# Kernel optimization log

Measured on AMD Instinct MI355X. Metric: run time of the kernel, lower is better.

## Reference

```python
import jax, jax.numpy as jnp
import numpy as np

B = 1024          # batch of positions
K = 64            # king squares
F = 640           # 64 squares * 10 piece types
C = 256           # accumulator channels


def setup_inputs() -> dict:
    key = jax.random.key(0)
    k1, k2, k3 = jax.random.split(key, 3)
    piece_positions = jax.random.randint(k1, (B, 64, 10), 0, 2).astype(jnp.bool_)
    king_positions = jax.random.randint(k2, (B, 2), 0, K, dtype=jnp.int32)
    input_weights = jax.random.normal(k3, (K, F + 1, C), dtype=jnp.float32)
    bias = jnp.zeros((C,), dtype=jnp.float32)
    return {
        "piece_positions": piece_positions,
        "king_positions": king_positions,
        "input_weights": input_weights,
        "bias": bias,
    }


def reference(piece_positions, king_positions, input_weights, bias):
    # Flatten the (64, 10) boolean piece plane into 640 HalfKP features.
    b = piece_positions.shape[0]
    p = piece_positions.reshape(b, F).astype(input_weights.dtype)          # (B, 640)
    # Gather each sample's white/black king weight slabs: (B, 2, 641, 256)
    Wg = jnp.take(input_weights, king_positions, axis=0)
    # Sparse-feature sum for both halves, contracted over feature dim and
    # summed over the two king perspectives in one einsum.
    halves = jnp.einsum("bf,bsfc->bc", p, Wg[:, :, :F, :])                 # (B, 256)
    extra = Wg[:, :, F, :].sum(axis=1)                                     # row 640 for each king
    return halves + extra + bias
```

## Files before the change

### kernel.cpp

```cpp
#include <hip/hip_runtime.h>
#include <hip/hip_bf16.h>


#define F_DIM 640
#define C_DIM 256
#define SLAB_STRIDE (641 * 256)
#define NKING 64
#define LCAP 256
#define NC_MAX 64
#define WPAD 36

#define WS_PART_OFF 0
#define WS_NEED (2 * 1024 * 256 * 4)

typedef float  f32x4  __attribute__((ext_vector_type(4)));
typedef short  bf16x8 __attribute__((ext_vector_type(8)));

__device__ __forceinline__ unsigned f2bf_pk(float a, float b) {
    union { float f; unsigned u; } x, y;
    x.f = a; y.f = b;
    const unsigned ra = (x.u + 0x7FFFu + ((x.u >> 16) & 1u)) >> 16;
    const unsigned rb = (y.u + 0x7FFFu + ((y.u >> 16) & 1u)) >> 16;
    return (ra & 0xFFFFu) | (rb << 16);
}

__device__ __forceinline__ bf16x8 mk_a8(unsigned m32, int g) {
    const unsigned by = (m32 >> (g * 8)) & 0xFFu;
    union { unsigned u[4]; bf16x8 v; } r;
    #pragma unroll
    for (int i = 0; i < 4; ++i)
        r.u[i] = (((by >> (2 * i)) & 1u) ? 0x3F80u : 0u) |
                 (((by >> (2 * i + 1)) & 1u) ? 0x3F800000u : 0u);
    return r.v;
}

__global__ __launch_bounds__(512, 4)
void halfkp_fused(const float* __restrict__ W,
                  const int* __restrict__ pieces,
                  const int* __restrict__ kings,
                  float* __restrict__ partial,
                  int nent)
{
    const int k  = blockIdx.x;
    const int cq = blockIdx.y;
    const int t  = threadIdx.x;
    const int wv = t >> 6, lane = t & 63;
    const int mt  = wv & 1;
    const int ntc = (wv >> 1) & 1;
    const int kh  = wv >> 2;
    const int li = lane & 15, g = lane >> 4;
    const int colL = ntc * 16 + li;
    const int colG = cq * 32 + colL;

    __shared__ unsigned s_W[336 * WPAD];
    __shared__ int s_ent[LCAP];
    __shared__ int s_cb[NC_MAX + 1];
    __shared__ unsigned s_m32[32][21];
    __shared__ f32x4 s_red[4][64];
    __shared__ int s_nk;

    const float* __restrict__ Wq = W + (size_t)k * SLAB_STRIDE + cq * 32;
    float4 ve[6], vo[6];
    #pragma unroll
    for (int it = 0; it < 6; ++it) {
        const int task = t + (it << 9);
        if (task < 336 * 8) {
            const int fp = task >> 3, c4 = task & 7;
            const int fe = min(2 * fp, F_DIM);
            const int fo = min(2 * fp + 1, F_DIM);
            ve[it] = *(const float4*)&Wq[(size_t)fe * C_DIM + c4 * 4];
            vo[it] = *(const float4*)&Wq[(size_t)fo * C_DIM + c4 * 4];
        }
    }

    {
        const int NC = nent >> 6;
        const int nit = NC >> 3;
        unsigned long long mm[8];
        #pragma unroll
        for (int it = 0; it < 8; ++it) {
            if (it < nit) {
                const int c = wv + (it << 3);
                const int kk = kings[(c << 6) + lane];
                mm[it] = __ballot(kk == k);
                if (lane == 0) s_cb[c] = (int)__popcll(mm[it]);
            }
        }
        __syncthreads();
        if (t == 0) {
            int s = 0;
            for (int c = 0; c < NC; ++c) { const int v = s_cb[c]; s_cb[c] = s; s += v; }
            s_nk = min(s, LCAP);
        }
        __syncthreads();
        const unsigned long long lt = (1ull << lane) - 1ull;
        #pragma unroll
        for (int it = 0; it < 8; ++it) {
            if (it < nit) {
                const int c = wv + (it << 3);
                if ((mm[it] >> lane) & 1ull) {
                    const int pos = s_cb[c] + (int)__popcll(mm[it] & lt);
                    if (pos < LCAP) s_ent[pos] = (c << 6) + lane;
                }
            }
        }
    }

    #pragma unroll
    for (int it = 0; it < 6; ++it) {
        const int task = t + (it << 9);
        if (task < 336 * 8) {
            const int fp = task >> 3, c4 = task & 7;
            union { unsigned u[4]; f32x4 v; } pk;
            pk.u[0] = f2bf_pk(ve[it].x, vo[it].x);
            pk.u[1] = f2bf_pk(ve[it].y, vo[it].y);
            pk.u[2] = f2bf_pk(ve[it].z, vo[it].z);
            pk.u[3] = f2bf_pk(ve[it].w, vo[it].w);
            *(f32x4*)&s_W[fp * WPAD + c4 * 4] = pk.v;
        }
    }
    __syncthreads();
    const int n_k = s_nk;

    for (int mb = 0; mb < n_k; mb += 32) {
        const int nc = min(n_k - mb, 32);

        int pv[4][10];
        #pragma unroll
        for (int j = 0; j < 4; ++j) {
            const int r = (wv << 2) + j;
            const int id = (r < nc) ? s_ent[mb + r] : -1;
            if (id >= 0) {
                const int* __restrict__ pb = pieces + (size_t)(id >> 1) * F_DIM;
                #pragma unroll
                for (int w2 = 0; w2 < 10; ++w2) pv[j][w2] = pb[w2 * 64 + lane];
            } else {
                #pragma unroll
                for (int w2 = 0; w2 < 10; ++w2) pv[j][w2] = 0;
            }
        }
        #pragma unroll
        for (int j = 0; j < 4; ++j) {
            const int r = (wv << 2) + j;
            const int id = (r < nc) ? s_ent[mb + r] : -1;
            #pragma unroll
            for (int w2 = 0; w2 < 10; ++w2) {
                const unsigned long long m64 = __ballot(pv[j][w2] != 0);
                if (lane == 0) {
                    s_m32[r][2 * w2]     = (unsigned)m64;
                    s_m32[r][2 * w2 + 1] = (unsigned)(m64 >> 32);
                }
            }
            if (lane == 0) s_m32[r][20] = (id >= 0) ? 1u : 0u;
        }
        __syncthreads();

        const unsigned* mrow = s_m32[mt * 16 + li];
        f32x4 acc = {0.f, 0.f, 0.f, 0.f};
        {
            const int ks_beg = kh ? 10 : 0;
            const int ks_end = kh ? 21 : 10;
            #pragma unroll 2
            for (int ks = ks_beg; ks < ks_end; ++ks) {
                const unsigned* bp = &s_W[(ks * 16 + g * 4) * WPAD + colL];
                union { unsigned u[4]; bf16x8 v; } bb;
                #pragma unroll
                for (int jj = 0; jj < 4; ++jj)
                    bb.u[jj] = bp[jj * WPAD];
                const bf16x8 af = mk_a8(mrow[ks], g);
                acc = __builtin_amdgcn_mfma_f32_16x16x32_bf16(af, bb.v, acc, 0, 0, 0);
            }
        }
        if (kh == 1) s_red[wv & 3][lane] = acc;
        __syncthreads();
        if (kh == 0) {
            acc += s_red[wv & 3][lane];
            #pragma unroll
            for (int i = 0; i < 4; ++i) {
                const int row = mt * 16 + 4 * g + i;
                if (row < nc) {
                    const int id = s_ent[mb + row];
                    partial[(((size_t)(id & 1)) * 1024 + (id >> 1)) * C_DIM + colG] = acc[i];
                }
            }
        }
        __syncthreads();
    }
}

__global__ __launch_bounds__(256)
void finalize(const float* __restrict__ partial,
              const float* __restrict__ bias,
              float* __restrict__ out)
{
    const int i = blockIdx.x * 256 + threadIdx.x;
    const float4 b4 = ((const float4*)bias)[i & 63];
    const float4 p0 = ((const float4*)partial)[i];
    const float4 p1 = ((const float4*)partial)[1024 * 64 + i];
    float4 o;
    o.x = b4.x + p0.x + p1.x;
    o.y = b4.y + p0.y + p1.y;
    o.z = b4.z + p0.z + p1.z;
    o.w = b4.w + p0.w + p1.w;
    ((float4*)out)[i] = o;
}

__global__ __launch_bounds__(256)
void halfkp_fallback(const int* __restrict__ pieces, const int* __restrict__ kings,
                     const float* __restrict__ W, const float* __restrict__ bias,
                     float* __restrict__ out)
{
    const int b = blockIdx.x;
    const int c = threadIdx.x;
    const int lane = c & 63;
    const int k0 = kings[2 * b + 0];
    const int k1 = kings[2 * b + 1];
    const float* W0 = W + (size_t)k0 * SLAB_STRIDE + c;
    const float* W1 = W + (size_t)k1 * SLAB_STRIDE + c;
    float acc = bias[c] + W0[640 * 256] + W1[640 * 256];
    const int* pi = pieces + (size_t)b * F_DIM;
    #pragma unroll
    for (int ch = 0; ch < 10; ++ch) {
        int v = pi[ch * 64 + lane];
        unsigned long long m = __ballot(v != 0);
        const float* b0 = W0 + ch * 64 * 256;
        const float* b1 = W1 + ch * 64 * 256;
        while (m) {
            const int f = __builtin_ctzll(m);
            m &= m - 1;
            acc += b0[f * 256] + b1[f * 256];
        }
    }
    out[(size_t)b * C_DIM + c] = acc;
}

extern "C" void kernel_launch(void* const* d_in, const int* in_sizes, int n_in,
                              void* d_out, int out_size, void* d_ws, size_t ws_size,
                              hipStream_t stream) {
    const int* pieces = (const int*)d_in[0];
    const int* kings  = (const int*)d_in[1];
    const float* W    = (const float*)d_in[2];
    const float* bias = (const float*)d_in[3];
    float* out        = (float*)d_out;

    const int B = in_sizes[1] / 2;
    const int nent = 2 * B;

    if (ws_size < (size_t)WS_NEED) {
        halfkp_fallback<<<dim3(B), dim3(C_DIM), 0, stream>>>(pieces, kings, W, bias, out);
        return;
    }

    float* part = (float*)((char*)d_ws + WS_PART_OFF);

    halfkp_fused<<<dim3(NKING, 8), dim3(512), 0, stream>>>(W, pieces, kings, part, nent);
    finalize<<<dim3(B * 64 / 256), dim3(256), 0, stream>>>(part, bias, out);
}
```

Before: 26.94 us.

## Replace partial buffer and finalize kernel with atomicAdd into zeroed output

Drops the two-slab partial workspace and the separate finalize kernel. The output is zeroed with a memset and each block atomically adds its per-perspective results, with bias folded in on the even perspective. It also skips MFMA work for wave row-halves that hold no live entries. This trades a kernel launch and the partial-buffer round trip for a memset plus global float atomics, which makes summation order nondeterministic.

```diff
diff --git a/kernel.cpp b/kernel.cpp
--- a/kernel.cpp
+++ b/kernel.cpp
@@ -9,9 +9,6 @@
 #define LCAP 256
 #define NC_MAX 64
 #define WPAD 36
-
-#define WS_PART_OFF 0
-#define WS_NEED (2 * 1024 * 256 * 4)
 
 typedef float  f32x4  __attribute__((ext_vector_type(4)));
 typedef short  bf16x8 __attribute__((ext_vector_type(8)));
@@ -38,7 +35,8 @@
 void halfkp_fused(const float* __restrict__ W,
                   const int* __restrict__ pieces,
                   const int* __restrict__ kings,
-                  float* __restrict__ partial,
+                  const float* __restrict__ bias,
+                  float* __restrict__ out,
                   int nent)
 {
     const int k  = blockIdx.x;
@@ -121,6 +119,7 @@
     }
     __syncthreads();
     const int n_k = s_nk;
+    const float bv = bias[colG];
 
     for (int mb = 0; mb < n_k; mb += 32) {
         const int nc = min(n_k - mb, 32);
@@ -155,9 +154,10 @@
         }
         __syncthreads();
 
-        const unsigned* mrow = s_m32[mt * 16 + li];
+        const bool live = (mt * 16) < nc;
         f32x4 acc = {0.f, 0.f, 0.f, 0.f};
-        {
+        if (live) {
+            const unsigned* mrow = s_m32[mt * 16 + li];
             const int ks_beg = kh ? 10 : 0;
             const int ks_end = kh ? 21 : 10;
             #pragma unroll 2
@@ -170,68 +170,23 @@
                 const bf16x8 af = mk_a8(mrow[ks], g);
                 acc = __builtin_amdgcn_mfma_f32_16x16x32_bf16(af, bb.v, acc, 0, 0, 0);
             }
-        }
-        if (kh == 1) s_red[wv & 3][lane] = acc;
-        __syncthreads();
-        if (kh == 0) {
+            if (kh == 1) s_red[wv & 3][lane] = acc;
+        }
+        __syncthreads();
+        if (live && kh == 0) {
             acc += s_red[wv & 3][lane];
             #pragma unroll
             for (int i = 0; i < 4; ++i) {
                 const int row = mt * 16 + 4 * g + i;
                 if (row < nc) {
                     const int id = s_ent[mb + row];
-                    partial[(((size_t)(id & 1)) * 1024 + (id >> 1)) * C_DIM + colG] = acc[i];
+                    const float val = acc[i] + (((id & 1) == 0) ? bv : 0.0f);
+                    atomicAdd(&out[(size_t)(id >> 1) * C_DIM + colG], val);
                 }
             }
         }
         __syncthreads();
     }
-}
-
-__global__ __launch_bounds__(256)
-void finalize(const float* __restrict__ partial,
-              const float* __restrict__ bias,
-              float* __restrict__ out)
-{
-    const int i = blockIdx.x * 256 + threadIdx.x;
-    const float4 b4 = ((const float4*)bias)[i & 63];
-    const float4 p0 = ((const float4*)partial)[i];
-    const float4 p1 = ((const float4*)partial)[1024 * 64 + i];
-    float4 o;
-    o.x = b4.x + p0.x + p1.x;
-    o.y = b4.y + p0.y + p1.y;
-    o.z = b4.z + p0.z + p1.z;
-    o.w = b4.w + p0.w + p1.w;
-    ((float4*)out)[i] = o;
-}
-
-__global__ __launch_bounds__(256)
-void halfkp_fallback(const int* __restrict__ pieces, const int* __restrict__ kings,
-                     const float* __restrict__ W, const float* __restrict__ bias,
-                     float* __restrict__ out)
-{
-    const int b = blockIdx.x;
-    const int c = threadIdx.x;
-    const int lane = c & 63;
-    const int k0 = kings[2 * b + 0];
-    const int k1 = kings[2 * b + 1];
-    const float* W0 = W + (size_t)k0 * SLAB_STRIDE + c;
-    const float* W1 = W + (size_t)k1 * SLAB_STRIDE + c;
-    float acc = bias[c] + W0[640 * 256] + W1[640 * 256];
-    const int* pi = pieces + (size_t)b * F_DIM;
-    #pragma unroll
-    for (int ch = 0; ch < 10; ++ch) {
-        int v = pi[ch * 64 + lane];
-        unsigned long long m = __ballot(v != 0);
-        const float* b0 = W0 + ch * 64 * 256;
-        const float* b1 = W1 + ch * 64 * 256;
-        while (m) {
-            const int f = __builtin_ctzll(m);
-            m &= m - 1;
-            acc += b0[f * 256] + b1[f * 256];
-        }
-    }
-    out[(size_t)b * C_DIM + c] = acc;
 }
 
 extern "C" void kernel_launch(void* const* d_in, const int* in_sizes, int n_in,
@@ -246,13 +201,6 @@
     const int B = in_sizes[1] / 2;
     const int nent = 2 * B;
 
-    if (ws_size < (size_t)WS_NEED) {
-        halfkp_fallback<<<dim3(B), dim3(C_DIM), 0, stream>>>(pieces, kings, W, bias, out);
-        return;
-    }
-
-    float* part = (float*)((char*)d_ws + WS_PART_OFF);
-
-    halfkp_fused<<<dim3(NKING, 8), dim3(512), 0, stream>>>(W, pieces, kings, part, nent);
-    finalize<<<dim3(B * 64 / 256), dim3(256), 0, stream>>>(part, bias, out);
-}
+    hipMemsetAsync(out, 0, (size_t)out_size * sizeof(float), stream);
+    halfkp_fused<<<dim3(NKING, 8), dim3(512), 0, stream>>>(W, pieces, kings, bias, out, nent);
+}
```

Measured after the change: 31.13 us. +15.5%, slower.
